# Kernel tuning notes

Hardware: AMD Instinct MI355X
Metric: run time of the kernel (lower is better)

Reference implementation:

```python
import jax, jax.numpy as jnp
import numpy as np

NUM_ROUTES = 8
TEMPERATURE = 0.1
NEG_INF = -1e9
EPS = 1e-12  # F.normalize eps


def _l2_normalize(t):
    n = jnp.sqrt(jnp.sum(t * t, axis=-1, keepdims=True))
    return t / jnp.maximum(n, EPS)


def setup_inputs() -> dict:
    key = jax.random.key(0)
    ks = jax.random.split(key, 7)
    B, P1, D = 4, 2049, 1024
    s = 1.0 / np.sqrt(D)
    return {
        "x": jax.random.normal(ks[0], (B, P1, D), jnp.float32),
        "Wq": jax.random.normal(ks[1], (D, D), jnp.float32) * s,
        "bq": jax.random.normal(ks[2], (D,), jnp.float32) * 0.01,
        "Wk": jax.random.normal(ks[3], (D, D), jnp.float32) * s,
        "bk": jax.random.normal(ks[4], (D,), jnp.float32) * 0.01,
        "Wv": jax.random.normal(ks[5], (D, D), jnp.float32) * s,
        "bv": jax.random.normal(ks[6], (D,), jnp.float32) * 0.01,
    }


def reference(x, Wq, bq, Wk, bk, Wv, bv):
    x = x[:, 1:, :]  # skip_first=True
    B, P, D = x.shape
    q = _l2_normalize(x @ Wq.T + bq)
    k = _l2_normalize(x @ Wk.T + bk)
    v = x @ Wv.T + bv
    scores = jnp.einsum('bpd,bqd->bpq', q, k)  # [B,P,P]
    diag = jnp.eye(P, dtype=bool)
    scores = jnp.where(diag[None], NEG_INF, scores)
    topk_scores, routes = jax.lax.top_k(scores / TEMPERATURE, NUM_ROUTES)  # [B,P,K]
    weights = jax.nn.softmax(topk_scores, axis=-1)
    b_idx = jnp.arange(B)[:, None, None]
    v_gathered = v[b_idx, routes]  # [B,P,K,D]
    features = jnp.einsum('bpk,bpkd->bpd', weights, v_gathered)
    return routes, weights, features
```

## Files before the change

kernel.cpp:

```cpp
#include <hip/hip_runtime.h>
#include <hip/hip_bf16.h>
#include <math.h>

#define TEMP 0.1
#define NC 12

typedef float f4 __attribute__((ext_vector_type(4)));
typedef short s8v __attribute__((ext_vector_type(8)));
typedef int   i4v __attribute__((ext_vector_type(4)));

__device__ inline short f2bf(float f) {
    __hip_bfloat16 h = __float2bfloat16(f);
    return *reinterpret_cast<short*>(&h);
}
__device__ inline float bf2f(short s) {
    __hip_bfloat16 h = *reinterpret_cast<__hip_bfloat16*>(&s);
    return __bfloat162float(h);
}

__global__ __launch_bounds__(256) void quantize_rows(
    const float* __restrict__ src, signed char* __restrict__ limbs,
    long plane_stride, double* __restrict__ scale)
{
    const int row = blockIdx.x, tid = threadIdx.x;
    const float4 v = ((const float4*)(src + (size_t)row * 1024))[tid];
    float m = fmaxf(fmaxf(fabsf(v.x), fabsf(v.y)), fmaxf(fabsf(v.z), fabsf(v.w)));
#pragma unroll
    for (int off = 32; off > 0; off >>= 1) m = fmaxf(m, __shfl_down(m, off));
    __shared__ float wmax[4];
    __shared__ int ssig;
    if ((tid & 63) == 0) wmax[tid >> 6] = m;
    __syncthreads();
    if (tid == 0) {
        float rm = fmaxf(fmaxf(wmax[0], wmax[1]), fmaxf(wmax[2], wmax[3]));
        int sig = (rm > 0.f) ? (29 - ilogbf(rm)) : 0;
        ssig = sig;
        scale[row] = ldexp(1.0, -sig);
    }
    __syncthreads();
    const double s2 = ldexp(1.0, ssig);
    float xs[4] = {v.x, v.y, v.z, v.w};
    signed char out[4][4];
#pragma unroll
    for (int e = 0; e < 4; ++e) {
        long X = __double2ll_rn((double)xs[e] * s2);
#pragma unroll
        for (int l = 0; l < 3; ++l) {
            int d = (int)(((X + 128) & 255) - 128);
            out[l][e] = (signed char)d;
            X = (X - d) >> 8;
        }
        out[3][e] = (signed char)X;
    }
#pragma unroll
    for (int l = 0; l < 4; ++l)
        *(char4*)&limbs[(size_t)l * plane_stride + (size_t)row * 1024 + tid * 4] =
            *(char4*)&out[l][0];
}

__global__ __launch_bounds__(256) void tobf16(
    const float* __restrict__ src, short* __restrict__ hi)
{
    const int row = blockIdx.x, tid = threadIdx.x;
    const float4 v = ((const float4*)(src + (size_t)row * 1024))[tid];
    __align__(8) short h[4] = {f2bf(v.x), f2bf(v.y), f2bf(v.z), f2bf(v.w)};
    *(short4*)&hi[(size_t)row * 1024 + tid * 4] = *(short4*)h;
}

__global__ __launch_bounds__(256) void prep_x(
    const float* __restrict__ src, signed char* __restrict__ limbs,
    long plane_stride, double* __restrict__ scale,
    short* __restrict__ hi)
{
    const int row = blockIdx.x, tid = threadIdx.x;
    const float4 v = ((const float4*)(src + (size_t)row * 1024))[tid];
    float m = fmaxf(fmaxf(fabsf(v.x), fabsf(v.y)), fmaxf(fabsf(v.z), fabsf(v.w)));
#pragma unroll
    for (int off = 32; off > 0; off >>= 1) m = fmaxf(m, __shfl_down(m, off));
    __shared__ float wmax[4];
    __shared__ int ssig;
    if ((tid & 63) == 0) wmax[tid >> 6] = m;
    __syncthreads();
    if (tid == 0) {
        float rm = fmaxf(fmaxf(wmax[0], wmax[1]), fmaxf(wmax[2], wmax[3]));
        int sig = (rm > 0.f) ? (29 - ilogbf(rm)) : 0;
        ssig = sig;
        scale[row] = ldexp(1.0, -sig);
    }
    __syncthreads();
    const double s2 = ldexp(1.0, ssig);
    float xs[4] = {v.x, v.y, v.z, v.w};
    signed char out[4][4];
    __align__(8) short h[4];
#pragma unroll
    for (int e = 0; e < 4; ++e) {
        long X = __double2ll_rn((double)xs[e] * s2);
#pragma unroll
        for (int lmb = 0; lmb < 3; ++lmb) {
            int d = (int)(((X + 128) & 255) - 128);
            out[lmb][e] = (signed char)d;
            X = (X - d) >> 8;
        }
        out[3][e] = (signed char)X;
        h[e] = f2bf(xs[e]);
    }
#pragma unroll
    for (int lmb = 0; lmb < 4; ++lmb)
        *(char4*)&limbs[(size_t)lmb * plane_stride + (size_t)row * 1024 + tid * 4] =
            *(char4*)&out[lmb][0];
    *(short4*)&hi[(size_t)row * 1024 + tid * 4] = *(short4*)h;
}

__global__ __launch_bounds__(256, 3) void gemm_i8qk(
    const signed char* __restrict__ Xl,
    const signed char* __restrict__ Wql,
    const signed char* __restrict__ Wkl,
    const double* __restrict__ xsc,
    const double* __restrict__ wqsc, const double* __restrict__ wksc,
    const float* __restrict__ bq, const float* __restrict__ bk,
    float* __restrict__ Qf, float* __restrict__ Kf)
{
    const int K = 1024, N = 1024;
    const long MK = 2048L * 1024, NK = 1024L * 1024;
    const signed char* Wl = blockIdx.z ? Wkl : Wql;
    const double* wsc = blockIdx.z ? wksc : wqsc;
    const float* bias = blockIdx.z ? bk : bq;
    float* C = blockIdx.z ? Kf : Qf;

    __shared__ __align__(16) signed char Asm[4][64][64];
    __shared__ __align__(16) signed char Bsm[4][64][64];

    const int tid  = threadIdx.x;
    const int lane = tid & 63, wave = tid >> 6;
    const int wm = wave >> 1, wn = wave & 1;
    const int quad = lane >> 4, l16 = lane & 15;
    const int m0 = blockIdx.y * 64, n0 = blockIdx.x * 64;

    const int srow = tid >> 2;
    const int cswz = ((tid & 3) ^ ((srow >> 1) & 3));
    const signed char* ap = Xl + (size_t)(m0 + srow) * K + cswz * 16;
    const signed char* bp = Wl + (size_t)(n0 + srow) * K + cswz * 16;

    i4v acc[4][2][2] = {};

    i4v at[4], bt[4];
#pragma unroll
    for (int l = 0; l < 4; ++l) {
        at[l] = *(const i4v*)(ap + l * MK);
        bt[l] = *(const i4v*)(bp + l * NK);
    }

    const int wpos = srow * 64 + (tid & 3) * 16;

    for (int k0 = 0; k0 < K; k0 += 64) {
        __syncthreads();
#pragma unroll
        for (int l = 0; l < 4; ++l) {
            *(i4v*)&Asm[l][0][wpos] = at[l];
            *(i4v*)&Bsm[l][0][wpos] = bt[l];
        }
        __syncthreads();

        if (k0 + 64 < K) {
#pragma unroll
            for (int l = 0; l < 4; ++l) {
                at[l] = *(const i4v*)(ap + l * MK + k0 + 64);
                bt[l] = *(const i4v*)(bp + l * NK + k0 + 64);
            }
        }

        i4v bF[4][2];
#pragma unroll
        for (int j = 0; j < 4; ++j)
#pragma unroll
            for (int nt = 0; nt < 2; ++nt) {
                const int R = wn * 32 + nt * 16 + l16;
                bF[j][nt] = *(const i4v*)&Bsm[j][R][(quad ^ ((R >> 1) & 3)) * 16];
            }

#pragma unroll
        for (int i = 0; i < 4; ++i) {
            const int R0 = wm * 32 + l16;
            const int R1 = wm * 32 + 16 + l16;
            i4v a0 = *(const i4v*)&Asm[i][R0][(quad ^ ((R0 >> 1) & 3)) * 16];
            i4v a1 = *(const i4v*)&Asm[i][R1][(quad ^ ((R1 >> 1) & 3)) * 16];
#pragma unroll
            for (int j = 0; j < 4; ++j) {
                if (i + j < 3) continue;
                const int s = i + j - 3;
                acc[s][0][0] = __builtin_amdgcn_mfma_i32_16x16x64_i8(a0, bF[j][0], acc[s][0][0], 0, 0, 0);
                acc[s][0][1] = __builtin_amdgcn_mfma_i32_16x16x64_i8(a0, bF[j][1], acc[s][0][1], 0, 0, 0);
                acc[s][1][0] = __builtin_amdgcn_mfma_i32_16x16x64_i8(a1, bF[j][0], acc[s][1][0], 0, 0, 0);
                acc[s][1][1] = __builtin_amdgcn_mfma_i32_16x16x64_i8(a1, bF[j][1], acc[s][1][1], 0, 0, 0);
            }
        }
    }

    const double wt0 = ldexp(1.0, 24), wt1 = ldexp(1.0, 32);
    const double wt2 = ldexp(1.0, 40), wt3 = ldexp(1.0, 48);
#pragma unroll
    for (int mt = 0; mt < 2; ++mt)
#pragma unroll
        for (int nt = 0; nt < 2; ++nt)
#pragma unroll
            for (int r = 0; r < 4; ++r) {
                int row = m0 + wm * 32 + mt * 16 + quad * 4 + r;
                int col = n0 + wn * 32 + nt * 16 + l16;
                double dsum = wt0 * (double)acc[0][mt][nt][r]
                            + wt1 * (double)acc[1][mt][nt][r]
                            + wt2 * (double)acc[2][mt][nt][r]
                            + wt3 * (double)acc[3][mt][nt][r];
                C[(size_t)row * N + col] =
                    (float)(dsum * xsc[row] * wsc[col] + (double)bias[col]);
            }
}

__global__ __launch_bounds__(256) void gemm_v64(
    const short* __restrict__ Ahp, const short* __restrict__ Bhp,
    const float* __restrict__ bias, float* __restrict__ C)
{
    const int K = 1024, N = 1024;
    __shared__ short Ah[64][40];
    __shared__ short Bh[64][40];

    const int tid = threadIdx.x, lane = tid & 63, wave = tid >> 6;
    const int wm = wave >> 1, wn = wave & 1;
    const int quad = lane >> 4, l16 = lane & 15;
    const int m0 = blockIdx.y * 64, n0 = blockIdx.x * 64;
    const int srow = tid >> 2, sco = (tid & 3) * 8;
    const size_t aoff = (size_t)(m0 + srow) * K + sco;
    const size_t boff = (size_t)(n0 + srow) * K + sco;

    f4 acc[2][2] = {};
    for (int k0 = 0; k0 < K; k0 += 32) {
        s8v ah = *(const s8v*)(Ahp + aoff + k0);
        s8v bh = *(const s8v*)(Bhp + boff + k0);
        __syncthreads();
        *(s8v*)&Ah[srow][sco] = ah;
        *(s8v*)&Bh[srow][sco] = bh;
        __syncthreads();

        s8v af[2], bf[2];
#pragma unroll
        for (int t = 0; t < 2; ++t) {
            af[t] = *(s8v*)&Ah[wm * 32 + t * 16 + l16][quad * 8];
            bf[t] = *(s8v*)&Bh[wn * 32 + t * 16 + l16][quad * 8];
        }
#pragma unroll
        for (int mt = 0; mt < 2; ++mt)
#pragma unroll
            for (int nt = 0; nt < 2; ++nt)
                acc[mt][nt] = __builtin_amdgcn_mfma_f32_16x16x32_bf16(
                    af[mt], bf[nt], acc[mt][nt], 0, 0, 0);
    }
#pragma unroll
    for (int mt = 0; mt < 2; ++mt)
#pragma unroll
        for (int nt = 0; nt < 2; ++nt)
#pragma unroll
            for (int r = 0; r < 4; ++r) {
                int row = m0 + wm * 32 + mt * 16 + quad * 4 + r;
                int col = n0 + wn * 32 + nt * 16 + l16;
                C[(size_t)row * N + col] = acc[mt][nt][r] + bias[col];
            }
}

__global__ __launch_bounds__(256) void gemm_score(
    const short* __restrict__ Qh, const short* __restrict__ Kh,
    float* __restrict__ C)
{
    const int K = 1024, N = 2048;
    __shared__ short As[64][40];
    __shared__ short Bs[64][40];
    const int tid = threadIdx.x, lane = tid & 63, wave = tid >> 6;
    const int wm = wave >> 1, wn = wave & 1;
    const int quad = lane >> 4, l16 = lane & 15;
    const int m0 = blockIdx.y * 64, n0 = blockIdx.x * 64;
    const int srow = tid >> 2, sco = (tid & 3) * 8;
    const short* ap = Qh + (size_t)(m0 + srow) * K + sco;
    const short* bp = Kh + (size_t)(n0 + srow) * K + sco;

    f4 acc[2][2] = {};
    for (int k0 = 0; k0 < K; k0 += 32) {
        s8v a8 = *(const s8v*)(ap + k0);
        s8v b8 = *(const s8v*)(bp + k0);
        __syncthreads();
        *(s8v*)&As[srow][sco] = a8;
        *(s8v*)&Bs[srow][sco] = b8;
        __syncthreads();
        s8v af[2], bf[2];
#pragma unroll
        for (int t = 0; t < 2; ++t) {
            af[t] = *(s8v*)&As[wm * 32 + t * 16 + l16][quad * 8];
            bf[t] = *(s8v*)&Bs[wn * 32 + t * 16 + l16][quad * 8];
        }
#pragma unroll
        for (int mt = 0; mt < 2; ++mt)
#pragma unroll
            for (int nt = 0; nt < 2; ++nt)
                acc[mt][nt] = __builtin_amdgcn_mfma_f32_16x16x32_bf16(
                    af[mt], bf[nt], acc[mt][nt], 0, 0, 0);
    }
#pragma unroll
    for (int mt = 0; mt < 2; ++mt)
#pragma unroll
        for (int nt = 0; nt < 2; ++nt)
#pragma unroll
            for (int r = 0; r < 4; ++r) {
                int row = m0 + wm * 32 + mt * 16 + quad * 4 + r;
                int col = n0 + wn * 32 + nt * 16 + l16;
                C[(size_t)row * N + col] = acc[mt][nt][r];
            }
}

__global__ __launch_bounds__(256) void l2norm_f32bf16(
    float* __restrict__ fq, float* __restrict__ fk,
    short* __restrict__ hq, short* __restrict__ hk)
{
    float* f = blockIdx.y ? fk : fq;
    short* h = blockIdx.y ? hk : hq;
    const int row = blockIdx.x;
    const int tid = threadIdx.x;
    float4* p4 = (float4*)(f + (size_t)row * 1024);
    float4 v = p4[tid];
    double s = (double)v.x * v.x + (double)v.y * v.y
             + (double)v.z * v.z + (double)v.w * v.w;
#pragma unroll
    for (int off = 32; off > 0; off >>= 1) s += __shfl_down(s, off);
    __shared__ double ws[5];
    if ((tid & 63) == 0) ws[tid >> 6] = s;
    __syncthreads();
    if (tid == 0) ws[4] = fmax(sqrt(ws[0] + ws[1] + ws[2] + ws[3]), 1e-12);
    __syncthreads();
    const double inv = 1.0 / ws[4];
    float o0 = (float)(v.x * inv), o1 = (float)(v.y * inv);
    float o2 = (float)(v.z * inv), o3 = (float)(v.w * inv);
    float4 o = make_float4(o0, o1, o2, o3);
    p4[tid] = o;
    __align__(8) short hv[4] = {f2bf(o0), f2bf(o1), f2bf(o2), f2bf(o3)};
    *(short4*)&h[(size_t)row * 1024 + tid * 4] = *(short4*)hv;
}

__global__ __launch_bounds__(256) void topk_route(
    const float*  __restrict__ S,
    const float*  __restrict__ Qf,
    const float*  __restrict__ Kf,
    const float*  __restrict__ Vf,
    float* __restrict__ routes_out,
    float* __restrict__ weights_out,
    float* __restrict__ feat_out,
    int batch)
{
    const int P = 2048, D = 1024;
    __shared__ float  qrow[1024];
    __shared__ float  cval[4 * NC];
    __shared__ int    cidx[4 * NC];
    __shared__ int    sel[NC];
    __shared__ double cscore[NC];
    __shared__ int    topi_s[8];
    __shared__ float  wts[8];

    const int p = blockIdx.x;
    const int tid = threadIdx.x;
    const int lane = tid & 63, wave = tid >> 6;

    const float4* sr4 = (const float4*)(S + (size_t)p * P);
    const float4 s0 = sr4[tid];
    const float4 s1 = sr4[tid + 256];
    ((float4*)qrow)[tid] = ((const float4*)(Qf + (size_t)p * D))[tid];

    float v[8] = {s0.x, s0.y, s0.z, s0.w, s1.x, s1.y, s1.z, s1.w};
    int   ji[8];
#pragma unroll
    for (int e = 0; e < 8; ++e) {
        ji[e] = (e < 4) ? (4 * tid + e) : (1024 + 4 * tid + (e - 4));
        if (ji[e] == p) v[e] = -1e30f;
    }

    float lv = v[0]; int li = ji[0];
#pragma unroll
    for (int e = 1; e < 8; ++e)
        if (v[e] > lv) { lv = v[e]; li = ji[e]; }

    float cv_ = -INFINITY; int ci_ = 0x7fffffff;
#pragma unroll 1
    for (int it = 0; it < NC; ++it) {
        float bv = lv; int bi = li;
#pragma unroll
        for (int off = 32; off > 0; off >>= 1) {
            float ov = __shfl_xor(bv, off);
            int   oi = __shfl_xor(bi, off);
            if (ov > bv || (ov == bv && oi < bi)) { bv = ov; bi = oi; }
        }
        if (lane == it) { cv_ = bv; ci_ = bi; }
#pragma unroll
        for (int e = 0; e < 8; ++e)
            if (ji[e] == bi) v[e] = -INFINITY;
        lv = v[0]; li = ji[0];
#pragma unroll
        for (int e = 1; e < 8; ++e)
            if (v[e] > lv) { lv = v[e]; li = ji[e]; }
    }
    if (lane < NC) { cval[wave * NC + lane] = cv_; cidx[wave * NC + lane] = ci_; }
    __syncthreads();

    if (wave == 0) {
        float mv = (lane < 4 * NC) ? cval[lane] : -INFINITY;
        int   mi = (lane < 4 * NC) ? cidx[lane] : 0x7fffffff;
        int rank = 0;
#pragma unroll 1
        for (int j = 0; j < 4 * NC; ++j) {
            float vj = __shfl(mv, j);
            int   ij = __shfl(mi, j);
            rank += (vj > mv || (vj == mv && ij < mi)) ? 1 : 0;
        }
        if (lane < 4 * NC && rank < NC) sel[rank] = mi;
    }
    __syncthreads();

    float pfv[NC];
#pragma unroll
    for (int c = 0; c < NC; ++c)
        pfv[c] = Vf[(size_t)sel[c] * D + tid * 4];

    {
        const float* k0r = Kf + (size_t)sel[wave] * D;
        const float* k1r = Kf + (size_t)sel[wave + 4] * D;
        const float* k2r = Kf + (size_t)sel[wave + 8] * D;
        double a0 = 0.0, a1 = 0.0, a2 = 0.0;
#pragma unroll 4
        for (int j = 0; j < 8; ++j) {
            const int e = lane * 2 + j * 128;
            const float2 q2 = *(const float2*)&qrow[e];
            const float2 kA = *(const float2*)&k0r[e];
            const float2 kB = *(const float2*)&k1r[e];
            const float2 kC = *(const float2*)&k2r[e];
            a0 = fma((double)q2.x, (double)kA.x, fma((double)q2.y, (double)kA.y, a0));
            a1 = fma((double)q2.x, (double)kB.x, fma((double)q2.y, (double)kB.y, a1));
            a2 = fma((double)q2.x, (double)kC.x, fma((double)q2.y, (double)kC.y, a2));
        }
#pragma unroll
        for (int off = 32; off > 0; off >>= 1) {
            a0 += __shfl_xor(a0, off);
            a1 += __shfl_xor(a1, off);
            a2 += __shfl_xor(a2, off);
        }
        if (lane == 0) {
            cscore[wave]     = a0;
            cscore[wave + 4] = a1;
            cscore[wave + 8] = a2;
        }
    }

    {
        float pf = 0.f;
#pragma unroll
        for (int c = 0; c < NC; ++c) pf += pfv[c];
        asm volatile("" :: "v"(pf));
    }
    __syncthreads();

    if (wave == 0) {
        double sc_ = (lane < NC) ? cscore[lane] : -1.0e308;
        int    id_ = (lane < NC) ? sel[lane]    : 0x7fffffff;
        int rank = 0;
#pragma unroll
        for (int j = 0; j < NC; ++j) {
            double vj = __shfl(sc_, j);
            int    ij = __shfl(id_, j);
            rank += (vj > sc_ || (vj == sc_ && ij < id_)) ? 1 : 0;
        }
        double mm = sc_;
#pragma unroll
        for (int off = 32; off > 0; off >>= 1) mm = fmax(mm, __shfl_xor(mm, off));
        double e = (rank < 8 && lane < NC) ? exp((sc_ - mm) / TEMP) : 0.0;
        double sum = e;
#pragma unroll
        for (int off = 32; off > 0; off >>= 1) sum += __shfl_xor(sum, off);
        if (rank < 8 && lane < NC) {
            float wk = (float)(e / sum);
            wts[rank] = wk; topi_s[rank] = id_;
            const size_t row = (size_t)batch * P + p;
            routes_out[row * 8 + rank]  = (float)id_;
            weights_out[row * 8 + rank] = wk;
        }
    }
    __syncthreads();

    float4 a = {0.f, 0.f, 0.f, 0.f};
#pragma unroll
    for (int k = 0; k < 8; ++k) {
        const float4 v4 = ((const float4*)(Vf + (size_t)topi_s[k] * D))[tid];
        float wk = wts[k];
        a.x = fmaf(wk, v4.x, a.x);
        a.y = fmaf(wk, v4.y, a.y);
        a.z = fmaf(wk, v4.z, a.z);
        a.w = fmaf(wk, v4.w, a.w);
    }
    ((float4*)(feat_out + ((size_t)batch * P + p) * D))[tid] = a;
}

extern "C" void kernel_launch(void* const* d_in, const int* in_sizes, int n_in,
                              void* d_out, int out_size, void* d_ws, size_t ws_size,
                              hipStream_t stream)
{
    const float* x  = (const float*)d_in[0];
    const float* Wq = (const float*)d_in[1];
    const float* bq = (const float*)d_in[2];
    const float* Wk = (const float*)d_in[3];
    const float* bk = (const float*)d_in[4];
    const float* Wv = (const float*)d_in[5];
    const float* bv = (const float*)d_in[6];

    const int B = 4, P = 2048, D = 1024;
    const size_t PD = (size_t)P * D;
    const size_t DD = (size_t)D * D;

    float*  Qf   = (float*)d_ws;
    float*  Kf   = Qf + PD;
    double* xsc  = (double*)(Kf + PD);
    double* wqsc = xsc + 2048;
    double* wksc = wqsc + 1024;
    short*  Qh   = (short*)(wksc + 1024);
    short*  Kh   = Qh + PD;
    short*  xh   = Kh + PD;
    short*  Wvh  = xh + PD;
    float*  Vf   = (float*)(Wvh + DD);
    float*  Sf   = Vf + PD;
    signed char* Xl  = (signed char*)(Sf + (size_t)P * P);
    signed char* Wql = Xl + 4 * PD;
    signed char* Wkl = Wql + 4 * DD;

    float* out     = (float*)d_out;
    float* routes  = out;
    float* weights = out + (size_t)B * P * 8;
    float* feat    = out + (size_t)B * P * 16;

    dim3 blk(256);
    quantize_rows<<<dim3(1024), blk, 0, stream>>>(Wq, Wql, (long)DD, wqsc);
    quantize_rows<<<dim3(1024), blk, 0, stream>>>(Wk, Wkl, (long)DD, wksc);
    tobf16<<<dim3(1024), blk, 0, stream>>>(Wv, Wvh);

    for (int b = 0; b < B; ++b) {
        const float* xb = x + ((size_t)b * 2049 + 1) * D;
        prep_x<<<dim3(P), blk, 0, stream>>>(xb, Xl, (long)PD, xsc, xh);
        gemm_i8qk<<<dim3(16, 32, 2), blk, 0, stream>>>(Xl, Wql, Wkl, xsc, wqsc, wksc,
                                                       bq, bk, Qf, Kf);
        gemm_v64<<<dim3(16, 32), blk, 0, stream>>>(xh, Wvh, bv, Vf);
        l2norm_f32bf16<<<dim3(P, 2), blk, 0, stream>>>(Qf, Kf, Qh, Kh);
        gemm_score<<<dim3(32, 32), blk, 0, stream>>>(Qh, Kh, Sf);
        topk_route<<<dim3(P), blk, 0, stream>>>(Sf, Qf, Kf, Vf, routes, weights, feat, b);
    }
}
```

Measured before the change: 724.8 us.

## Load GEMM tiles directly into LDS with global_load_lds and swizzled layout

Replaces register-staged global-to-shared copies in the int8 QK GEMM, V GEMM and score GEMM with direct global-to-LDS loads (16-byte buffer loads into LDS). The padded shared tiles become unpadded with an XOR swizzle to avoid bank conflicts, and launch bounds are raised to 4 blocks per CU. The aim is fewer VGPRs and LDS write instructions and higher occupancy. In exchange, the int8 kernel loses its register prefetch of the next tile, so loads are no longer overlapped with compute except through occupancy.

```diff
diff --git a/kernel.cpp b/kernel.cpp
--- a/kernel.cpp
+++ b/kernel.cpp
@@ -16,6 +16,12 @@
 __device__ inline float bf2f(short s) {
     __hip_bfloat16 h = *reinterpret_cast<__hip_bfloat16*>(&s);
     return __bfloat162float(h);
+}
+
+__device__ __forceinline__ void g2l16(const void* g, void* l) {
+    __builtin_amdgcn_global_load_lds(
+        (const __attribute__((address_space(1))) void*)g,
+        (__attribute__((address_space(3))) void*)l, 16, 0, 0);
 }
 
 __global__ __launch_bounds__(256) void quantize_rows(
@@ -111,7 +117,7 @@
     *(short4*)&hi[(size_t)row * 1024 + tid * 4] = *(short4*)h;
 }
 
-__global__ __launch_bounds__(256, 3) void gemm_i8qk(
+__global__ __launch_bounds__(256, 4) void gemm_i8qk(
     const signed char* __restrict__ Xl,
     const signed char* __restrict__ Wql,
     const signed char* __restrict__ Wkl,
@@ -141,33 +147,19 @@
     const signed char* ap = Xl + (size_t)(m0 + srow) * K + cswz * 16;
     const signed char* bp = Wl + (size_t)(n0 + srow) * K + cswz * 16;
 
+    signed char* aw = (signed char*)Asm + (wave << 10);
+    signed char* bw = (signed char*)Bsm + (wave << 10);
+
     i4v acc[4][2][2] = {};
-
-    i4v at[4], bt[4];
-#pragma unroll
-    for (int l = 0; l < 4; ++l) {
-        at[l] = *(const i4v*)(ap + l * MK);
-        bt[l] = *(const i4v*)(bp + l * NK);
-    }
-
-    const int wpos = srow * 64 + (tid & 3) * 16;
 
     for (int k0 = 0; k0 < K; k0 += 64) {
         __syncthreads();
 #pragma unroll
         for (int l = 0; l < 4; ++l) {
-            *(i4v*)&Asm[l][0][wpos] = at[l];
-            *(i4v*)&Bsm[l][0][wpos] = bt[l];
+            g2l16(ap + l * MK + k0, aw + l * 4096);
+            g2l16(bp + l * NK + k0, bw + l * 4096);
         }
         __syncthreads();
-
-        if (k0 + 64 < K) {
-#pragma unroll
-            for (int l = 0; l < 4; ++l) {
-                at[l] = *(const i4v*)(ap + l * MK + k0 + 64);
-                bt[l] = *(const i4v*)(bp + l * NK + k0 + 64);
-            }
-        }
 
         i4v bF[4][2];
 #pragma unroll
@@ -215,36 +207,39 @@
             }
 }
 
-__global__ __launch_bounds__(256) void gemm_v64(
+__global__ __launch_bounds__(256, 4) void gemm_v64(
     const short* __restrict__ Ahp, const short* __restrict__ Bhp,
     const float* __restrict__ bias, float* __restrict__ C)
 {
     const int K = 1024, N = 1024;
-    __shared__ short Ah[64][40];
-    __shared__ short Bh[64][40];
+    __shared__ __align__(16) short Ah[64][32];
+    __shared__ __align__(16) short Bh[64][32];
 
     const int tid = threadIdx.x, lane = tid & 63, wave = tid >> 6;
     const int wm = wave >> 1, wn = wave & 1;
     const int quad = lane >> 4, l16 = lane & 15;
     const int m0 = blockIdx.y * 64, n0 = blockIdx.x * 64;
-    const int srow = tid >> 2, sco = (tid & 3) * 8;
-    const size_t aoff = (size_t)(m0 + srow) * K + sco;
-    const size_t boff = (size_t)(n0 + srow) * K + sco;
+    const int srow = tid >> 2;
+    const int cswz = ((tid & 3) ^ ((srow >> 1) & 3));
+    const char* ap = (const char*)(Ahp + (size_t)(m0 + srow) * K) + cswz * 16;
+    const char* bp = (const char*)(Bhp + (size_t)(n0 + srow) * K) + cswz * 16;
+    char* aw = (char*)Ah + (wave << 10);
+    char* bw = (char*)Bh + (wave << 10);
 
     f4 acc[2][2] = {};
     for (int k0 = 0; k0 < K; k0 += 32) {
-        s8v ah = *(const s8v*)(Ahp + aoff + k0);
-        s8v bh = *(const s8v*)(Bhp + boff + k0);
         __syncthreads();
-        *(s8v*)&Ah[srow][sco] = ah;
-        *(s8v*)&Bh[srow][sco] = bh;
+        g2l16(ap + 2 * k0, aw);
+        g2l16(bp + 2 * k0, bw);
         __syncthreads();
 
         s8v af[2], bf[2];
 #pragma unroll
         for (int t = 0; t < 2; ++t) {
-            af[t] = *(s8v*)&Ah[wm * 32 + t * 16 + l16][quad * 8];
-            bf[t] = *(s8v*)&Bh[wn * 32 + t * 16 + l16][quad * 8];
+            const int Ra = wm * 32 + t * 16 + l16;
+            const int Rb = wn * 32 + t * 16 + l16;
+            af[t] = *(const s8v*)((const char*)Ah + Ra * 64 + ((quad ^ ((Ra >> 1) & 3)) << 4));
+            bf[t] = *(const s8v*)((const char*)Bh + Rb * 64 + ((quad ^ ((Rb >> 1) & 3)) << 4));
         }
 #pragma unroll
         for (int mt = 0; mt < 2; ++mt)
@@ -265,34 +260,38 @@
             }
 }
 
-__global__ __launch_bounds__(256) void gemm_score(
+__global__ __launch_bounds__(256, 4) void gemm_score(
     const short* __restrict__ Qh, const short* __restrict__ Kh,
     float* __restrict__ C)
 {
     const int K = 1024, N = 2048;
-    __shared__ short As[64][40];
-    __shared__ short Bs[64][40];
+    __shared__ __align__(16) short As[64][32];
+    __shared__ __align__(16) short Bs[64][32];
     const int tid = threadIdx.x, lane = tid & 63, wave = tid >> 6;
     const int wm = wave >> 1, wn = wave & 1;
     const int quad = lane >> 4, l16 = lane & 15;
     const int m0 = blockIdx.y * 64, n0 = blockIdx.x * 64;
-    const int srow = tid >> 2, sco = (tid & 3) * 8;
-    const short* ap = Qh + (size_t)(m0 + srow) * K + sco;
-    const short* bp = Kh + (size_t)(n0 + srow) * K + sco;
+    const int srow = tid >> 2;
+    const int cswz = ((tid & 3) ^ ((srow >> 1) & 3));
+    const char* ap = (const char*)(Qh + (size_t)(m0 + srow) * K) + cswz * 16;
+    const char* bp = (const char*)(Kh + (size_t)(n0 + srow) * K) + cswz * 16;
+    char* aw = (char*)As + (wave << 10);
+    char* bw = (char*)Bs + (wave << 10);
 
     f4 acc[2][2] = {};
     for (int k0 = 0; k0 < K; k0 += 32) {
-        s8v a8 = *(const s8v*)(ap + k0);
-        s8v b8 = *(const s8v*)(bp + k0);
         __syncthreads();
-        *(s8v*)&As[srow][sco] = a8;
-        *(s8v*)&Bs[srow][sco] = b8;
+        g2l16(ap + 2 * k0, aw);
+        g2l16(bp + 2 * k0, bw);
         __syncthreads();
+
         s8v af[2], bf[2];
 #pragma unroll
         for (int t = 0; t < 2; ++t) {
-            af[t] = *(s8v*)&As[wm * 32 + t * 16 + l16][quad * 8];
-            bf[t] = *(s8v*)&Bs[wn * 32 + t * 16 + l16][quad * 8];
+            const int Ra = wm * 32 + t * 16 + l16;
+            const int Rb = wn * 32 + t * 16 + l16;
+            af[t] = *(const s8v*)((const char*)As + Ra * 64 + ((quad ^ ((Ra >> 1) & 3)) << 4));
+            bf[t] = *(const s8v*)((const char*)Bs + Rb * 64 + ((quad ^ ((Rb >> 1) & 3)) << 4));
         }
 #pragma unroll
         for (int mt = 0; mt < 2; ++mt)
```

Measured after the change: 662.7 us. 8.6% less time.
